# Kernel optimization log

Hardware: AMD Instinct MI355X
Metric: run time of the kernel (lower is better)

## Reference

```python
import jax, jax.numpy as jnp
import numpy as np

N = 50000       # nodes
E = 1600000     # edges (avg degree 32)
DIN = 64
DOUT = 64
DE = 16
ATT_SLOPE = 0.2   # leaky_relu slope inside attention (GAT standard)
ACT_SLOPE = 0.01  # F.leaky_relu default between layers


def setup_inputs() -> dict:
    key = jax.random.key(0)
    ks = jax.random.split(key, 16)

    def lin(k, i, o):
        return jax.random.normal(k, (i, o), jnp.float32) / np.sqrt(i).astype(np.float32)

    def vec(k, d):
        return jax.random.normal(k, (d,), jnp.float32) / np.sqrt(d).astype(np.float32)

    return {
        "X": jax.random.normal(ks[0], (N, DIN), jnp.float32),
        "edge_index": jax.random.randint(ks[1], (2, E), 0, N),
        "edge_attr": jax.random.normal(ks[2], (E, DE), jnp.float32),
        # layer 1 params
        "W1": lin(ks[3], DIN, DOUT), "We1": lin(ks[4], DE, DOUT),
        "as1": vec(ks[5], DOUT), "ad1": vec(ks[6], DOUT), "ae1": vec(ks[7], DOUT),
        "b1": jnp.zeros((DOUT,), jnp.float32),
        # layer 2 params
        "W2": lin(ks[8], DOUT, DOUT), "We2": lin(ks[9], DE, DOUT),
        "as2": vec(ks[10], DOUT), "ad2": vec(ks[11], DOUT), "ae2": vec(ks[12], DOUT),
        "b2": jnp.zeros((DOUT,), jnp.float32),
    }


def _gat_conv(x, src, dst, edge_attr, W, We, a_s, a_d, a_e, b):
    """GATConv with edge features, softmax attention over dst neighborhoods, max aggregation."""
    n = x.shape[0]
    h = x @ W                      # [N, DOUT]
    e = edge_attr @ We             # [E, DOUT]
    # per-edge attention logits
    logits = jax.nn.leaky_relu((h @ a_s)[src] + (h @ a_d)[dst] + e @ a_e, ATT_SLOPE)  # [E]
    # numerically-stable segment softmax over destination node
    m = jax.ops.segment_max(logits, dst, num_segments=n)      # [N]
    p = jnp.exp(logits - m[dst])                               # [E]
    s = jax.ops.segment_sum(p, dst, num_segments=n)            # [N]
    att = p / jnp.maximum(s[dst], 1e-16)                       # [E]
    msg = (h[src] + e) * att[:, None]                          # [E, DOUT]
    out = jax.ops.segment_max(msg, dst, num_segments=n)        # [N, DOUT], -inf for empty
    out = jnp.where(jnp.isfinite(out), out, 0.0)
    return out + b


def reference(X, edge_index, edge_attr,
              W1, We1, as1, ad1, ae1, b1,
              W2, We2, as2, ad2, ae2, b2):
    src, dst = edge_index[0], edge_index[1]
    c1 = _gat_conv(X, src, dst, edge_attr, W1, We1, as1, ad1, ae1, b1)
    c1 = jax.nn.leaky_relu(c1, ACT_SLOPE)
    c2 = _gat_conv(c1, src, dst, edge_attr, W2, We2, as2, ad2, ae2, b2)
    c2 = jax.nn.leaky_relu(c2, ACT_SLOPE)
    return c2
```

## Files before the change

### kernel.cpp

```cpp
#include <hip/hip_runtime.h>
#include <cstdint>
#include <cstddef>

#define NN 50000
#define EE 1600000
#define D  64
#define DE 16

typedef __attribute__((ext_vector_type(2))) float vf2;

__device__ __forceinline__ float bf2f(unsigned short u) {
    return __uint_as_float(((unsigned)u) << 16);
}
__device__ __forceinline__ unsigned short f2bf(float f) {
    unsigned u = __float_as_uint(f);
    unsigned r = u + 0x7FFFu + ((u >> 16) & 1u);
    return (unsigned short)(r >> 16);
}

__global__ __launch_bounds__(256) void k_hist(const int* dst, int* counts) {
    int e = blockIdx.x * 256 + threadIdx.x;
    if (e < EE) atomicAdd(&counts[dst[e]], 1);
}

__global__ __launch_bounds__(256) void k_scanA(const int* counts, int* bsum) {
    __shared__ int tmp[256];
    int t = threadIdx.x, i = blockIdx.x * 256 + t;
    tmp[t] = (i < NN) ? counts[i] : 0;
    __syncthreads();
    for (int off = 128; off; off >>= 1) {
        if (t < off) tmp[t] += tmp[t + off];
        __syncthreads();
    }
    if (t == 0) bsum[blockIdx.x] = tmp[0];
}

__global__ __launch_bounds__(256) void k_scanB(int* bsum, int nchunks,
                                               const float* We1, const float* ae1,
                                               const float* We2, const float* ae2,
                                               float* wae) {
    __shared__ int tmp[256];
    int t = threadIdx.x;
    int v = (t < nchunks) ? bsum[t] : 0;
    tmp[t] = v; __syncthreads();
    for (int off = 1; off < 256; off <<= 1) {
        int x = (t >= off) ? tmp[t - off] : 0;
        __syncthreads();
        tmp[t] += x;
        __syncthreads();
    }
    if (t < nchunks) bsum[t] = tmp[t] - v;
    if (t < 32) {
        const float* We = (t < 16) ? We1 : We2;
        const float* ae = (t < 16) ? ae1 : ae2;
        int k = t & 15;
        float acc = 0.f;
        #pragma unroll
        for (int c = 0; c < 64; c++) acc += We[k * 64 + c] * ae[c];
        wae[t] = acc;
    }
}

__global__ __launch_bounds__(256) void k_scanC(const int* counts, const int* bsumex,
                                               int* offsets, int* cursor) {
    __shared__ int tmp[256];
    int t = threadIdx.x, i = blockIdx.x * 256 + t;
    int v = (i < NN) ? counts[i] : 0;
    tmp[t] = v; __syncthreads();
    for (int off = 1; off < 256; off <<= 1) {
        int x = (t >= off) ? tmp[t - off] : 0;
        __syncthreads();
        tmp[t] += x;
        __syncthreads();
    }
    int excl = tmp[t] - v + bsumex[blockIdx.x];
    if (i < NN) { offsets[i] = excl; cursor[i] = excl; }
}

#define SC_ILP 8
__global__ __launch_bounds__(256) void k_scatter(const int* __restrict__ src,
                                                 const int* __restrict__ dst,
                                                 int* __restrict__ cursor,
                                                 int2* __restrict__ recs) {
    int t = threadIdx.x;
    int base = blockIdx.x * (256 * SC_ILP) + t;
    int dd[SC_ILP], ss[SC_ILP], pos[SC_ILP];
    bool v[SC_ILP];
    #pragma unroll
    for (int j = 0; j < SC_ILP; j++) {
        int e = base + j * 256;
        v[j] = (e < EE);
        int ec = v[j] ? e : 0;
        dd[j] = dst[ec];
        ss[j] = src[ec];
    }
    #pragma unroll
    for (int j = 0; j < SC_ILP; j++)
        if (v[j]) pos[j] = atomicAdd(&cursor[dd[j]], 1);
    #pragma unroll
    for (int j = 0; j < SC_ILP; j++)
        if (v[j]) recs[pos[j]] = make_int2(ss[j], base + j * 256);
}

template<int IN_BF16>
__global__ __launch_bounds__(256, 4) void k_gemm(const void* xin, const float* W,
                                                 const float* a_s, const float* a_d,
                                                 unsigned short* h, float* hs, float* hd) {
    int t = threadIdx.x, lane = t & 63;
    int wid0 = blockIdx.x * 4 + (t >> 6);
    float Wcol[64];
    #pragma unroll
    for (int k = 0; k < 64; k++) Wcol[k] = W[k * 64 + lane];
    float asl = a_s[lane], adl = a_d[lane];
    for (int n0 = wid0; n0 < NN; n0 += 4096) {
        int n = __builtin_amdgcn_readfirstlane(n0);
        float acc = 0.f;
        if (IN_BF16) {
            const uint4* xr = (const uint4*)((const unsigned short*)xin + (size_t)n * 64);
            #pragma unroll
            for (int q = 0; q < 8; q++) {
                uint4 u = xr[q];
                unsigned uu[4] = {u.x, u.y, u.z, u.w};
                #pragma unroll
                for (int j = 0; j < 4; j++) {
                    acc += bf2f((unsigned short)(uu[j] & 0xFFFFu)) * Wcol[q * 8 + 2 * j];
                    acc += bf2f((unsigned short)(uu[j] >> 16))     * Wcol[q * 8 + 2 * j + 1];
                }
            }
        } else {
            const float4* xr = (const float4*)((const float*)xin + (size_t)n * 64);
            #pragma unroll
            for (int q = 0; q < 16; q++) {
                float4 u = xr[q];
                acc += u.x * Wcol[4 * q]     + u.y * Wcol[4 * q + 1]
                     + u.z * Wcol[4 * q + 2] + u.w * Wcol[4 * q + 3];
            }
        }
        h[(size_t)n * 64 + lane] = f2bf(acc);
        float ps = acc * asl, pd = acc * adl;
        #pragma unroll
        for (int off = 32; off; off >>= 1) {
            ps += __shfl_xor(ps, off);
            pd += __shfl_xor(pd, off);
        }
        if (lane == 0) { hs[n] = ps; hd[n] = pd; }
    }
}

template<int L2>
__global__ __launch_bounds__(256, 3) void k_gat(const int2* __restrict__ recs,
                                                const int* __restrict__ offsets,
                                                const int* __restrict__ counts,
                                                const float* __restrict__ hs,
                                                const float* __restrict__ hd,
                                                const unsigned short* __restrict__ h,
                                                const float* __restrict__ ea,
                                                const float* __restrict__ wae,
                                                const float* __restrict__ We,
                                                const float* __restrict__ b,
                                                void* __restrict__ outv) {
    __shared__ float4 eal[4][4][64];
    __shared__ __align__(16) unsigned short hl[4][64][64];
    __shared__ float attl[4][64];
    int t = threadIdx.x, lane = t & 63, wv = t >> 6;
    int g = lane >> 4, cl = lane & 15;

    vf2 Wp[32];
    #pragma unroll
    for (int kp = 0; kp < 8; kp++) {
        float4 wa = *(const float4*)(We + (2 * kp) * 64 + 4 * cl);
        float4 wb = *(const float4*)(We + (2 * kp + 1) * 64 + 4 * cl);
        Wp[kp].x      = wa.x; Wp[kp].y      = wb.x;
        Wp[8 + kp].x  = wa.y; Wp[8 + kp].y  = wb.y;
        Wp[16 + kp].x = wa.z; Wp[16 + kp].y = wb.z;
        Wp[24 + kp].x = wa.w; Wp[24 + kp].y = wb.w;
    }
    float waer[16];
    {
        const float4* wp4 = (const float4*)(wae + L2 * 16);
        float4 w0 = wp4[0], w1 = wp4[1], w2 = wp4[2], w3 = wp4[3];
        waer[0]=w0.x; waer[1]=w0.y; waer[2]=w0.z; waer[3]=w0.w;
        waer[4]=w1.x; waer[5]=w1.y; waer[6]=w1.z; waer[7]=w1.w;
        waer[8]=w2.x; waer[9]=w2.y; waer[10]=w2.z; waer[11]=w2.w;
        waer[12]=w3.x; waer[13]=w3.y; waer[14]=w3.z; waer[15]=w3.w;
    }

    int d = blockIdx.x * 4 + wv;
    int start = offsets[d];
    int deg = counts[d];

    if (deg == 0) {
        if (g == 0) {
            float4 bl = *(const float4*)(b + 4 * cl);
            float o0 = (bl.x >= 0.f) ? bl.x : 0.01f * bl.x;
            float o1 = (bl.y >= 0.f) ? bl.y : 0.01f * bl.y;
            float o2 = (bl.z >= 0.f) ? bl.z : 0.01f * bl.z;
            float o3 = (bl.w >= 0.f) ? bl.w : 0.01f * bl.w;
            size_t oidx = (size_t)d * D + 4 * cl;
            if (L2) *(float4*)((float*)outv + oidx) = make_float4(o0, o1, o2, o3);
            else {
                ushort4 ov = {f2bf(o0), f2bf(o1), f2bf(o2), f2bf(o3)};
                *(ushort4*)((unsigned short*)outv + oidx) = ov;
            }
        }
        return;
    }

    float hdv = hd[d];
    bool fast = (deg <= 64);
    float m, invs;

    float ninf = -__builtin_inff();
    float a0 = ninf, a1 = ninf, a2 = ninf, a3 = ninf;

    if (fast) {
        float lg = ninf;
        if (lane < deg) {
            int2 r = recs[start + lane];
            int sr = r.x, eid = r.y;
            const float4* ep = (const float4*)(ea + (size_t)eid * DE);
            float4 q0 = ep[0], q1 = ep[1], q2 = ep[2], q3 = ep[3];
            const uint4* hp = (const uint4*)(h + (size_t)sr * D);
            float hsv = hs[sr];
            eal[wv][0][lane] = q0; eal[wv][1][lane] = q1;
            eal[wv][2][lane] = q2; eal[wv][3][lane] = q3;
            #pragma unroll
            for (int q = 0; q < 8; q++) {
                uint4 hvq = hp[q];
                *(uint4*)&hl[wv][lane][(8 * q) ^ ((lane & 7) << 3)] = hvq;
            }
            float ev[16] = {q0.x, q0.y, q0.z, q0.w, q1.x, q1.y, q1.z, q1.w,
                            q2.x, q2.y, q2.z, q2.w, q3.x, q3.y, q3.z, q3.w};
            float ee = 0.f;
            #pragma unroll
            for (int j = 0; j < 16; j++) ee += ev[j] * waer[j];
            lg = hsv + hdv + ee;
            lg = (lg >= 0.f) ? lg : 0.2f * lg;
        }

        m = lg;
        #pragma unroll
        for (int off = 32; off; off >>= 1) m = fmaxf(m, __shfl_xor(m, off));
        float p = __expf(lg - m);
        float s = p;
        #pragma unroll
        for (int off = 32; off; off >>= 1) s += __shfl_xor(s, off);
        invs = 1.0f / fmaxf(s, 1e-16f);
        if (lane < deg) attl[wv][lane] = p * invs;

        bool vC = (g < deg);
        int jC = vC ? g : 0;
        float4 qA[4];
        #pragma unroll
        for (int kq = 0; kq < 4; kq++) qA[kq] = eal[wv][kq][jC];
        ushort4 hC = *(const ushort4*)&hl[wv][jC][(4 * cl) ^ ((jC & 7) << 3)];
        float attC = attl[wv][jC];

        for (int i = 0; i < deg; i += 4) {
            int jn = i + 4 + g;
            bool vN = (jn < deg);
            int jN = vN ? jn : 0;
            float4 qB[4];
            #pragma unroll
            for (int kq = 0; kq < 4; kq++) qB[kq] = eal[wv][kq][jN];
            ushort4 hN = *(const ushort4*)&hl[wv][jN][(4 * cl) ^ ((jN & 7) << 3)];
            float attN = attl[wv][jN];

            vf2 acA = {0.f, 0.f}, acB = {0.f, 0.f}, acC2 = {0.f, 0.f}, acD = {0.f, 0.f};
            #pragma unroll
            for (int kq = 0; kq < 4; kq++) {
                float4 q = qA[kq];
                vf2 eA; eA.x = q.x; eA.y = q.y;
                vf2 eB; eB.x = q.z; eB.y = q.w;
                acA += eA * Wp[2 * kq];       acA += eB * Wp[2 * kq + 1];
                acB += eA * Wp[8 + 2 * kq];   acB += eB * Wp[8 + 2 * kq + 1];
                acC2 += eA * Wp[16 + 2 * kq]; acC2 += eB * Wp[16 + 2 * kq + 1];
                acD += eA * Wp[24 + 2 * kq];  acD += eB * Wp[24 + 2 * kq + 1];
            }
            float e0 = acA.x + acA.y, e1 = acB.x + acB.y;
            float e2 = acC2.x + acC2.y, e3 = acD.x + acD.y;
            float o0 = (bf2f(hC.x) + e0) * attC;
            float o1 = (bf2f(hC.y) + e1) * attC;
            float o2 = (bf2f(hC.z) + e2) * attC;
            float o3 = (bf2f(hC.w) + e3) * attC;
            if (vC) {
                a0 = fmaxf(a0, o0); a1 = fmaxf(a1, o1);
                a2 = fmaxf(a2, o2); a3 = fmaxf(a3, o3);
            }
            #pragma unroll
            for (int kq = 0; kq < 4; kq++) qA[kq] = qB[kq];
            hC = hN; attC = attN; vC = vN;
        }
    } else {
        float mm = ninf, s = 0.f;
        for (int i = lane; i < deg; i += 64) {
            int2 r = recs[start + i];
            const float4* ep = (const float4*)(ea + (size_t)r.y * DE);
            float4 q0 = ep[0], q1 = ep[1], q2 = ep[2], q3 = ep[3];
            float ev[16] = {q0.x, q0.y, q0.z, q0.w, q1.x, q1.y, q1.z, q1.w,
                            q2.x, q2.y, q2.z, q2.w, q3.x, q3.y, q3.z, q3.w};
            float ee = 0.f;
            #pragma unroll
            for (int j = 0; j < 16; j++) ee += ev[j] * waer[j];
            float lg = hs[r.x] + hdv + ee;
            lg = (lg >= 0.f) ? lg : 0.2f * lg;
            float mn = fmaxf(mm, lg);
            s = ((mm == mn) ? s : s * __expf(mm - mn)) + __expf(lg - mn);
            mm = mn;
        }
        #pragma unroll
        for (int off = 32; off; off >>= 1) {
            float m2 = __shfl_xor(mm, off);
            float s2 = __shfl_xor(s, off);
            float mn = fmaxf(mm, m2);
            float sa = (mm == mn) ? s : s * __expf(mm - mn);
            float sb = (m2 == mn) ? s2 : s2 * __expf(m2 - mn);
            s = sa + sb;
            mm = mn;
        }
        m = mm;
        invs = 1.0f / fmaxf(s, 1e-16f);

        for (int i = 0; i < deg; i += 4) {
            int j = i + g;
            bool valid = (j < deg);
            int jc = valid ? j : 0;
            int2 r = recs[start + jc];
            const float4* ep = (const float4*)(ea + (size_t)r.y * DE);
            float4 q0 = ep[0], q1 = ep[1], q2 = ep[2], q3 = ep[3];
            float ev[16] = {q0.x, q0.y, q0.z, q0.w, q1.x, q1.y, q1.z, q1.w,
                            q2.x, q2.y, q2.z, q2.w, q3.x, q3.y, q3.z, q3.w};
            float ee = 0.f;
            #pragma unroll
            for (int j2 = 0; j2 < 16; j2++) ee += ev[j2] * waer[j2];
            float lg = hs[r.x] + hdv + ee;
            lg = (lg >= 0.f) ? lg : 0.2f * lg;
            float att = __expf(lg - m) * invs;
            ushort4 hv = *(const ushort4*)(h + (size_t)r.x * D + 4 * cl);
            float4 qs[4] = {q0, q1, q2, q3};
            vf2 acA = {0.f, 0.f}, acB = {0.f, 0.f}, acC2 = {0.f, 0.f}, acD = {0.f, 0.f};
            #pragma unroll
            for (int kq = 0; kq < 4; kq++) {
                float4 q = qs[kq];
                vf2 eA; eA.x = q.x; eA.y = q.y;
                vf2 eB; eB.x = q.z; eB.y = q.w;
                acA += eA * Wp[2 * kq];       acA += eB * Wp[2 * kq + 1];
                acB += eA * Wp[8 + 2 * kq];   acB += eB * Wp[8 + 2 * kq + 1];
                acC2 += eA * Wp[16 + 2 * kq]; acC2 += eB * Wp[16 + 2 * kq + 1];
                acD += eA * Wp[24 + 2 * kq];  acD += eB * Wp[24 + 2 * kq + 1];
            }
            float e0 = acA.x + acA.y, e1 = acB.x + acB.y;
            float e2 = acC2.x + acC2.y, e3 = acD.x + acD.y;
            float o0 = (bf2f(hv.x) + e0) * att;
            float o1 = (bf2f(hv.y) + e1) * att;
            float o2 = (bf2f(hv.z) + e2) * att;
            float o3 = (bf2f(hv.w) + e3) * att;
            if (valid) {
                a0 = fmaxf(a0, o0); a1 = fmaxf(a1, o1);
                a2 = fmaxf(a2, o2); a3 = fmaxf(a3, o3);
            }
        }
    }

    #pragma unroll
    for (int off = 16; off <= 32; off <<= 1) {
        a0 = fmaxf(a0, __shfl_xor(a0, off));
        a1 = fmaxf(a1, __shfl_xor(a1, off));
        a2 = fmaxf(a2, __shfl_xor(a2, off));
        a3 = fmaxf(a3, __shfl_xor(a3, off));
    }

    if (g == 0) {
        float4 bl = *(const float4*)(b + 4 * cl);
        float o0 = a0 + bl.x, o1 = a1 + bl.y;
        float o2 = a2 + bl.z, o3 = a3 + bl.w;
        o0 = (o0 >= 0.f) ? o0 : 0.01f * o0;
        o1 = (o1 >= 0.f) ? o1 : 0.01f * o1;
        o2 = (o2 >= 0.f) ? o2 : 0.01f * o2;
        o3 = (o3 >= 0.f) ? o3 : 0.01f * o3;
        size_t oidx = (size_t)d * D + 4 * cl;
        if (L2) {
            *(float4*)((float*)outv + oidx) = make_float4(o0, o1, o2, o3);
        } else {
            ushort4 ov = {f2bf(o0), f2bf(o1), f2bf(o2), f2bf(o3)};
            *(ushort4*)((unsigned short*)outv + oidx) = ov;
        }
    }
}

extern "C" void kernel_launch(void* const* d_in, const int* in_sizes, int n_in,
                              void* d_out, int out_size, void* d_ws, size_t ws_size,
                              hipStream_t stream) {
    const float* X   = (const float*)d_in[0];
    const int*   eix = (const int*)d_in[1];
    const float* ea  = (const float*)d_in[2];
    const float* W1  = (const float*)d_in[3];
    const float* We1 = (const float*)d_in[4];
    const float* as1 = (const float*)d_in[5];
    const float* ad1 = (const float*)d_in[6];
    const float* ae1 = (const float*)d_in[7];
    const float* b1  = (const float*)d_in[8];
    const float* W2  = (const float*)d_in[9];
    const float* We2 = (const float*)d_in[10];
    const float* as2 = (const float*)d_in[11];
    const float* ad2 = (const float*)d_in[12];
    const float* ae2 = (const float*)d_in[13];
    const float* b2  = (const float*)d_in[14];

    const int* src = eix;
    const int* dst = eix + EE;

    char* w = (char*)d_ws;
    int2* recs = (int2*)w;               w += (size_t)EE * 8;
    unsigned short* hA = (unsigned short*)w; w += (size_t)NN * D * 2;
    unsigned short* hB = (unsigned short*)w; w += (size_t)NN * D * 2;
    float* hs = (float*)w;               w += (size_t)NN * 4;
    float* hd = (float*)w;               w += (size_t)NN * 4;
    int* counts = (int*)w;               w += (size_t)NN * 4;
    int* offsets = (int*)w;              w += (size_t)NN * 4;
    int* cursor = (int*)w;               w += (size_t)NN * 4;
    int* bsum = (int*)w;                 w += 256 * 4;
    float* wae = (float*)w;              w += 32 * 4;

    const int nchunks = (NN + 255) / 256;
    const int nsblk = (EE + 2047) / 2048;

    hipMemsetAsync(counts, 0, (size_t)NN * 4, stream);
    k_hist<<<(EE + 255) / 256, 256, 0, stream>>>(dst, counts);
    k_scanA<<<nchunks, 256, 0, stream>>>(counts, bsum);
    k_scanB<<<1, 256, 0, stream>>>(bsum, nchunks, We1, ae1, We2, ae2, wae);
    k_scanC<<<nchunks, 256, 0, stream>>>(counts, bsum, offsets, cursor);
    k_scatter<<<nsblk, 256, 0, stream>>>(src, dst, cursor, recs);

    k_gemm<0><<<1024, 256, 0, stream>>>(X, W1, as1, ad1, hA, hs, hd);
    k_gat<0><<<NN / 4, 256, 0, stream>>>(recs, offsets, counts, hs, hd, hA, ea,
                                         wae, We1, b1, hB);
    k_gemm<1><<<1024, 256, 0, stream>>>(hB, W2, as2, ad2, hB, hs, hd);
    k_gat<1><<<NN / 4, 256, 0, stream>>>(recs, offsets, counts, hs, hd, hB, ea,
                                         wae, We2, b2, (float*)d_out);
}
```

Baseline: 620.6 us.

## Gather neighbor rows directly from global in GAT fast path; add ILP to histogram

In the fast path of the GAT kernel, neighbor feature rows are no longer staged into a large shared-memory tile. Each 16-lane group now loads its ushort4 slice of the neighbor row straight from global memory, one neighbor ahead, using the source id kept in a small shared array next to the attention weight. This cuts LDS use per block and the staging pass, which may raise occupancy, but it exposes global gather latency inside the aggregation loop. Separately, the degree histogram kernel now has each thread handle four edges, with the loads issued before the atomics. The scatter grid is now sized from an SC_ILP constant.

```diff
diff --git a/kernel.cpp b/kernel.cpp
--- a/kernel.cpp
+++ b/kernel.cpp
@@ -18,9 +18,20 @@
     return (unsigned short)(r >> 16);
 }
 
-__global__ __launch_bounds__(256) void k_hist(const int* dst, int* counts) {
-    int e = blockIdx.x * 256 + threadIdx.x;
-    if (e < EE) atomicAdd(&counts[dst[e]], 1);
+#define HI_ILP 4
+__global__ __launch_bounds__(256) void k_hist(const int* __restrict__ dst,
+                                              int* __restrict__ counts) {
+    int base = blockIdx.x * (256 * HI_ILP) + threadIdx.x;
+    int dd[HI_ILP]; bool v[HI_ILP];
+    #pragma unroll
+    for (int j = 0; j < HI_ILP; j++) {
+        int e = base + j * 256;
+        v[j] = (e < EE);
+        dd[j] = dst[v[j] ? e : 0];
+    }
+    #pragma unroll
+    for (int j = 0; j < HI_ILP; j++)
+        if (v[j]) atomicAdd(&counts[dd[j]], 1);
 }
 
 __global__ __launch_bounds__(256) void k_scanA(const int* counts, int* bsum) {
@@ -160,8 +171,7 @@
                                                 const float* __restrict__ b,
                                                 void* __restrict__ outv) {
     __shared__ float4 eal[4][4][64];
-    __shared__ __align__(16) unsigned short hl[4][64][64];
-    __shared__ float attl[4][64];
+    __shared__ float2 arx[4][64];
     int t = threadIdx.x, lane = t & 63, wv = t >> 6;
     int g = lane >> 4, cl = lane & 15;
 
@@ -217,18 +227,12 @@
         float lg = ninf;
         if (lane < deg) {
             int2 r = recs[start + lane];
-            int sr = r.x, eid = r.y;
-            const float4* ep = (const float4*)(ea + (size_t)eid * DE);
+            const float4* ep = (const float4*)(ea + (size_t)r.y * DE);
             float4 q0 = ep[0], q1 = ep[1], q2 = ep[2], q3 = ep[3];
-            const uint4* hp = (const uint4*)(h + (size_t)sr * D);
-            float hsv = hs[sr];
+            float hsv = hs[r.x];
             eal[wv][0][lane] = q0; eal[wv][1][lane] = q1;
             eal[wv][2][lane] = q2; eal[wv][3][lane] = q3;
-            #pragma unroll
-            for (int q = 0; q < 8; q++) {
-                uint4 hvq = hp[q];
-                *(uint4*)&hl[wv][lane][(8 * q) ^ ((lane & 7) << 3)] = hvq;
-            }
+            arx[wv][lane].y = __int_as_float(r.x);
             float ev[16] = {q0.x, q0.y, q0.z, q0.w, q1.x, q1.y, q1.z, q1.w,
                             q2.x, q2.y, q2.z, q2.w, q3.x, q3.y, q3.z, q3.w};
             float ee = 0.f;
@@ -237,6 +241,11 @@
             lg = hsv + hdv + ee;
             lg = (lg >= 0.f) ? lg : 0.2f * lg;
         }
+
+        bool vC = (g < deg);
+        int jC = vC ? g : 0;
+        int rxC = __float_as_int(arx[wv][jC].y);
+        ushort4 hvC = *(const ushort4*)(h + (size_t)rxC * D + 4 * cl);
 
         m = lg;
         #pragma unroll
@@ -246,30 +255,22 @@
         #pragma unroll
         for (int off = 32; off; off >>= 1) s += __shfl_xor(s, off);
         invs = 1.0f / fmaxf(s, 1e-16f);
-        if (lane < deg) attl[wv][lane] = p * invs;
-
-        bool vC = (g < deg);
-        int jC = vC ? g : 0;
-        float4 qA[4];
-        #pragma unroll
-        for (int kq = 0; kq < 4; kq++) qA[kq] = eal[wv][kq][jC];
-        ushort4 hC = *(const ushort4*)&hl[wv][jC][(4 * cl) ^ ((jC & 7) << 3)];
-        float attC = attl[wv][jC];
+        if (lane < deg) arx[wv][lane].x = p * invs;
+
+        float attC = arx[wv][jC].x;
 
         for (int i = 0; i < deg; i += 4) {
             int jn = i + 4 + g;
             bool vN = (jn < deg);
             int jN = vN ? jn : 0;
-            float4 qB[4];
-            #pragma unroll
-            for (int kq = 0; kq < 4; kq++) qB[kq] = eal[wv][kq][jN];
-            ushort4 hN = *(const ushort4*)&hl[wv][jN][(4 * cl) ^ ((jN & 7) << 3)];
-            float attN = attl[wv][jN];
+            float2 arN = arx[wv][jN];
+            int rxN = __float_as_int(arN.y);
+            ushort4 hvN = *(const ushort4*)(h + (size_t)rxN * D + 4 * cl);
 
             vf2 acA = {0.f, 0.f}, acB = {0.f, 0.f}, acC2 = {0.f, 0.f}, acD = {0.f, 0.f};
             #pragma unroll
             for (int kq = 0; kq < 4; kq++) {
-                float4 q = qA[kq];
+                float4 q = eal[wv][kq][jC];
                 vf2 eA; eA.x = q.x; eA.y = q.y;
                 vf2 eB; eB.x = q.z; eB.y = q.w;
                 acA += eA * Wp[2 * kq];       acA += eB * Wp[2 * kq + 1];
@@ -279,17 +280,15 @@
             }
             float e0 = acA.x + acA.y, e1 = acB.x + acB.y;
             float e2 = acC2.x + acC2.y, e3 = acD.x + acD.y;
-            float o0 = (bf2f(hC.x) + e0) * attC;
-            float o1 = (bf2f(hC.y) + e1) * attC;
-            float o2 = (bf2f(hC.z) + e2) * attC;
-            float o3 = (bf2f(hC.w) + e3) * attC;
+            float o0 = (bf2f(hvC.x) + e0) * attC;
+            float o1 = (bf2f(hvC.y) + e1) * attC;
+            float o2 = (bf2f(hvC.z) + e2) * attC;
+            float o3 = (bf2f(hvC.w) + e3) * attC;
             if (vC) {
                 a0 = fmaxf(a0, o0); a1 = fmaxf(a1, o1);
                 a2 = fmaxf(a2, o2); a3 = fmaxf(a3, o3);
             }
-            #pragma unroll
-            for (int kq = 0; kq < 4; kq++) qA[kq] = qB[kq];
-            hC = hN; attC = attN; vC = vN;
+            attC = arN.x; hvC = hvN; vC = vN; jC = jN;
         }
     } else {
         float mm = ninf, s = 0.f;
@@ -423,10 +422,11 @@
     float* wae = (float*)w;              w += 32 * 4;
 
     const int nchunks = (NN + 255) / 256;
-    const int nsblk = (EE + 2047) / 2048;
+    const int nhblk = (EE + 256 * HI_ILP - 1) / (256 * HI_ILP);
+    const int nsblk = (EE + 256 * SC_ILP - 1) / (256 * SC_ILP);
 
     hipMemsetAsync(counts, 0, (size_t)NN * 4, stream);
-    k_hist<<<(EE + 255) / 256, 256, 0, stream>>>(dst, counts);
+    k_hist<<<nhblk, 256, 0, stream>>>(dst, counts);
     k_scanA<<<nchunks, 256, 0, stream>>>(counts, bsum);
     k_scanB<<<1, 256, 0, stream>>>(bsum, nchunks, We1, ae1, We2, ae2, wae);
     k_scanC<<<nchunks, 256, 0, stream>>>(counts, bsum, offsets, cursor);
```

Result: no change. 614.7 us (-0.9%).
